# Optimization experiments

Hardware: AMD Instinct MI355X
Metric: run time of the kernel (lower is better)

## Reference

```python
import jax, jax.numpy as jnp
import numpy as np

H = 50      # hidden_size (fixed in source)
IN = 7      # input_size = len(features)
B = 1024    # batch
T = 512     # seq_len
FC1 = 25
OUT = 1


def setup_inputs() -> dict:
    key = jax.random.key(0)
    ks = jax.random.split(key, 24)
    s = 1.0 / np.sqrt(H)  # PyTorch LSTM/Linear default uniform init scale

    def u(k, shape):
        return jax.random.uniform(k, shape, jnp.float32, -s, s)

    d = {"x": jax.random.normal(ks[0], (B, T, IN), jnp.float32)}
    # 4 stacked LSTM layers total: lstm1 has 2 layers (in=7 then 50), lstm2 has 2 layers (in=50)
    in_sizes = [IN, H, H, H]
    for l, isz in enumerate(in_sizes):
        d[f"Wih{l}"] = u(ks[1 + 4 * l], (4 * H, isz))
        d[f"Whh{l}"] = u(ks[2 + 4 * l], (4 * H, H))
        d[f"bih{l}"] = u(ks[3 + 4 * l], (4 * H,))
        d[f"bhh{l}"] = u(ks[4 + 4 * l], (4 * H,))
    d["W1"] = u(ks[17], (FC1, H))
    d["b1"] = u(ks[18], (FC1,))
    d["W2"] = u(ks[19], (OUT, FC1))
    d["b2"] = u(ks[20], (OUT,))
    return d


def _lstm_layer(x, Wih, Whh, bih, bhh):
    # x: [B, T, in] -> hidden sequence [B, T, H]. PyTorch gate order: i, f, g, o.
    b, t, _ = x.shape
    h = Whh.shape[1]
    # Precompute input projection for all timesteps in one big GEMM: [T, B, 4H]
    xp = jnp.einsum('bti,gi->tbg', x, Wih) + (bih + bhh)

    def step(carry, xt):
        hs, cs = carry
        gates = xt + hs @ Whh.T                      # [B, 4H]
        i, f, g, o = jnp.split(gates, 4, axis=-1)
        i = jax.nn.sigmoid(i)
        f = jax.nn.sigmoid(f)
        g = jnp.tanh(g)
        o = jax.nn.sigmoid(o)
        cs = f * cs + i * g
        hs = o * jnp.tanh(cs)
        return (hs, cs), hs

    h0 = jnp.zeros((b, h), x.dtype)
    _, hseq = jax.lax.scan(step, (h0, h0), xp)       # hseq: [T, B, H]
    return hseq.transpose(1, 0, 2)


def reference(x, Wih0, Whh0, bih0, bhh0, Wih1, Whh1, bih1, bhh1,
              Wih2, Whh2, bih2, bhh2, Wih3, Whh3, bih3, bhh3,
              W1, b1, W2, b2):
    out = x
    layers = [(Wih0, Whh0, bih0, bhh0), (Wih1, Whh1, bih1, bhh1),
              (Wih2, Whh2, bih2, bhh2), (Wih3, Whh3, bih3, bhh3)]
    for Wih, Whh, bih, bhh in layers:
        out = _lstm_layer(out, Wih, Whh, bih, bhh)
    h = out[:, -1, :]                                # last timestep [B, H]
    # dropout is identity in eval mode
    h = jax.nn.relu(h @ W1.T + b1)
    return h @ W2.T + b2                             # [B, 1]
```

## Files before the change

### kernel.cpp

```cpp
#include <hip/hip_runtime.h>


#define H 50
#define INSZ 7
#define TT 512
#define NL 4
#define FC1N 25
#define BPG 4
#define NBLK 256
#define NTHREADS 1024
#define HS 80
#define BIASL 56

typedef _Float16 half_t;
typedef __attribute__((ext_vector_type(8))) _Float16 half8_t;
typedef __attribute__((ext_vector_type(4))) float float4_t;

struct Params {
  const float* x;
  const float* Wih[NL];
  const float* Whh[NL];
  const float* bih[NL];
  const float* bhh[NL];
  const float* W1;
  const float* b1;
  const float* W2;
  const float* b2;
  float* out;
};

#define MFMA16(A, B, C) __builtin_amdgcn_mfma_f32_16x16x32_f16((A), (B), (C), 0, 0, 0)
#define EXP2F(x) __builtin_amdgcn_exp2f(x)
#define RCPF(x) __builtin_amdgcn_rcpf(x)

__global__ __launch_bounds__(NTHREADS, 4) void lstm_r13(Params p) {
  __shared__ __align__(16) half_t XP[3][BPG][HS];
  __shared__ __align__(16) half_t Hb[3][3][BPG][HS];
  __shared__ __align__(16) half_t Xstage[32][BPG][8];
  __shared__ int prodc[16];
  __shared__ float fc1_buf[BPG][FC1N];

  const int tid = threadIdx.x;
  const int b0 = blockIdx.x * BPG;
  const int lane = tid & 63;
  const int quad = lane >> 4;
  const int col = lane & 15;
  const int glay = tid >> 8;
  const int wl = (((tid >> 6) & 3) + glay) & 3;

  half8_t afrag[4][4];
#pragma unroll
  for (int t4 = 0; t4 < 4; ++t4) {
#pragma unroll
    for (int g = 0; g < 4; ++g) {
      half8_t v;
#pragma unroll
      for (int j = 0; j < 8; ++j) {
        const int r = wl * 64 + t4 * 16 + col;
        const int u = r >> 2, q = r & 3;
        const int k = g * 32 + quad * 8 + j;
        float wv = 0.0f;
        if (u < H) {
          const int row = q * H + u;
          if (glay == 0) {
            if (k < INSZ) wv = p.Wih[0][row * INSZ + k];
            else if (k == 7) wv = p.bih[0][row] + p.bhh[0][row];
            else if (k >= 8 && k < 8 + H) wv = p.Whh[0][row * H + (k - 8)];
          } else if (glay == 1) {
            if (k == 7) wv = p.bih[1][row] + p.bhh[1][row];
            else if (k >= 8 && k < 8 + H) wv = p.Wih[1][row * H + (k - 8)];
            else if (k >= 64 && k < 64 + H) wv = p.Whh[1][row * H + (k - 64)];
          } else {
            if (k < H) wv = p.Wih[glay][row * H + k];
            else if (k == BIASL) wv = p.bih[glay][row] + p.bhh[glay][row];
            else if (k >= 64 && k < 64 + H) wv = p.Whh[glay][row * H + (k - 64)];
          }
          wv *= (q == 2) ? -2.885390082f : -1.442695041f;
        }
        v[j] = (half_t)wv;
      }
      afrag[t4][g] = v;
    }
  }

  {
    unsigned* xz = (unsigned*)XP;
    for (int i = tid; i < 3 * BPG * HS / 2; i += NTHREADS) xz[i] = 0u;
    unsigned* hz = (unsigned*)Hb;
    for (int i = tid; i < 3 * 3 * BPG * HS / 2; i += NTHREADS) hz[i] = 0u;
    if (tid < 16) prodc[tid] = 0;
  }
  __syncthreads();
  if (tid < 12) {
    XP[tid >> 2][tid & 3][7] = (half_t)1.0f;
  } else if (tid < 12 + 36) {
    const int i = tid - 12, l = i / 12, pr = (i >> 2) % 3, b = i & 3;
    Hb[l][pr][b][BIASL] = (half_t)1.0f;
  }
  for (int i = tid; i < 32 * BPG * INSZ; i += NTHREADS) {
    const int t = i / (BPG * INSZ), rem = i % (BPG * INSZ);
    const int b = rem / INSZ, k = rem % INSZ;
    const half_t xh = (half_t)p.x[((size_t)(b0 + b) * TT + t) * INSZ + k];
    Xstage[t][b][k] = xh;
    if (t == 0) XP[2][b][k] = xh;
  }
  __syncthreads();

  const int bb = col & 3;
  const int tsel = col >> 2;
  const int uu = 16 * wl + 4 * tsel + quad;
  const bool updact = (uu < H);

  const half_t* pin3[3];
  const half_t* pown3[3];
  half_t* pst3[3];
#pragma unroll
  for (int pp = 0; pp < 3; ++pp) {
    if (glay == 0) {
      pin3[pp] = &XP[pp][bb][quad * 8];
      pown3[pp] = pin3[pp];
      pst3[pp] = &XP[pp][bb][8 + uu];
    } else if (glay == 1) {
      pin3[pp] = &XP[pp][bb][quad * 8];
      pown3[pp] = &Hb[0][pp][bb][quad * 8];
      pst3[pp] = &Hb[0][pp][bb][uu];
    } else {
      pin3[pp] = &Hb[glay - 2][pp][bb][quad * 8];
      pown3[pp] = &Hb[glay - 1][pp][bb][quad * 8];
      pst3[pp] = &Hb[glay - 1][pp][bb][uu];
    }
  }
  const half_t* pinT[3] = {glay ? pin3[0] : pin3[2],
                           glay ? pin3[1] : pin3[0],
                           glay ? pin3[2] : pin3[1]};
  const half_t* pownT[3] = {pown3[2], pown3[0], pown3[1]};

  const bool xwave = (glay == 0) && (wl == 3);
  const bool xcopy = xwave && (lane < BPG * INSZ);
  const int cb = lane / INSZ, ck = lane % INSZ;

  float cst = 0.0f;
  const float4_t fzc = {0.0f, 0.0f, 0.0f, 0.0f};
  volatile int* pv = (volatile int*)prodc;

#define WAITT(T_)                                                               \
  {                                                                             \
    const int bS = 4 * (T_);                                                    \
    if (glay == 0) {                                                            \
      while (pv[0] < bS || pv[1] < bS - 4) {}                                   \
    } else if (glay == 1) {                                                     \
      while (pv[1] < bS || pv[0] < bS + 4 || pv[2] < bS - 4) {}                 \
    } else if (glay == 2) {                                                     \
      while (pv[2] < bS || pv[1] < bS + 4 || pv[3] < bS - 4) {}                 \
    } else {                                                                    \
      while (pv[3] < bS || pv[2] < bS + 4) {}                                   \
    }                                                                           \
    __builtin_amdgcn_sched_barrier(0);                                          \
    asm volatile("" ::: "memory");                                              \
  }

#define DONE()                                                                  \
  {                                                                             \
    asm volatile("s_waitcnt lgkmcnt(0)" ::: "memory");                          \
    if (lane == 0) atomicAdd(&prodc[glay], 1);                                  \
  }

#define REFILL(T_)                                                              \
  if (xwave && ((T_)&15) == 0 && (T_) > 0 && (T_) + 16 < TT) {                  \
    const int t0 = (T_) + 16 + (lane >> 2);                                     \
    const int rb = lane & 3;                                                    \
    const float* src = &p.x[((size_t)(b0 + rb) * TT + t0) * INSZ];              \
    half_t* dst = &Xstage[t0 & 31][rb][0];                                      \
    _Pragma("unroll") for (int k = 0; k < INSZ; ++k) dst[k] = (half_t)src[k];   \
  }

#define TICK3(PIN, POWN, PST)                                                   \
  {                                                                             \
    float4_t a0, a1, a2, a3;                                                    \
    if (glay == 0) {                                                            \
      const half8_t v0 = *(const half8_t*)(PIN);                                \
      const half8_t v1 = *(const half8_t*)((PIN) + 32);                         \
      __builtin_amdgcn_s_setprio(1);                                            \
      if (wl != 3) {                                                            \
        a0 = MFMA16(afrag[0][0], v0, fzc); a1 = MFMA16(afrag[1][0], v0, fzc);   \
        a2 = MFMA16(afrag[2][0], v0, fzc); a3 = MFMA16(afrag[3][0], v0, fzc);   \
        a0 = MFMA16(afrag[0][1], v1, a0); a1 = MFMA16(afrag[1][1], v1, a1);     \
        a2 = MFMA16(afrag[2][1], v1, a2); a3 = MFMA16(afrag[3][1], v1, a3);     \
      } else {                                                                  \
        a0 = MFMA16(afrag[0][0], v0, fzc);                                      \
        a0 = MFMA16(afrag[0][1], v1, a0);                                       \
        a1 = a0; a2 = a0; a3 = a0;                                              \
      }                                                                         \
      __builtin_amdgcn_s_setprio(0);                                            \
    } else {                                                                    \
      const half8_t v0 = *(const half8_t*)(PIN);                                \
      const half8_t v1 = *(const half8_t*)((PIN) + 32);                         \
      const half8_t v2 = *(const half8_t*)(POWN);                               \
      const half8_t v3 = *(const half8_t*)((POWN) + 32);                        \
      __builtin_amdgcn_s_setprio(1);                                            \
      if (wl != 3) {                                                            \
        a0 = MFMA16(afrag[0][0], v0, fzc); a1 = MFMA16(afrag[1][0], v0, fzc);   \
        a2 = MFMA16(afrag[2][0], v0, fzc); a3 = MFMA16(afrag[3][0], v0, fzc);   \
        a0 = MFMA16(afrag[0][1], v1, a0); a1 = MFMA16(afrag[1][1], v1, a1);     \
        a2 = MFMA16(afrag[2][1], v1, a2); a3 = MFMA16(afrag[3][1], v1, a3);     \
        a0 = MFMA16(afrag[0][2], v2, a0); a1 = MFMA16(afrag[1][2], v2, a1);     \
        a2 = MFMA16(afrag[2][2], v2, a2); a3 = MFMA16(afrag[3][2], v2, a3);     \
        a0 = MFMA16(afrag[0][3], v3, a0); a1 = MFMA16(afrag[1][3], v3, a1);     \
        a2 = MFMA16(afrag[2][3], v3, a2); a3 = MFMA16(afrag[3][3], v3, a3);     \
      } else {                                                                  \
        a0 = MFMA16(afrag[0][0], v0, fzc);                                      \
        a0 = MFMA16(afrag[0][1], v1, a0);                                       \
        a0 = MFMA16(afrag[0][2], v2, a0);                                       \
        a0 = MFMA16(afrag[0][3], v3, a0);                                       \
        a1 = a0; a2 = a0; a3 = a0;                                              \
      }                                                                         \
      __builtin_amdgcn_s_setprio(0);                                            \
    }                                                                           \
    if (updact) {                                                               \
      const float4_t g01 = (col & 4) ? a1 : a0;                                 \
      const float4_t g23 = (col & 4) ? a3 : a2;                                 \
      const float4_t ga = (col & 8) ? g23 : g01;                                \
      const float di = 1.0f + EXP2F(ga[0]);                                     \
      const float df = 1.0f + EXP2F(ga[1]);                                     \
      const float dg = 1.0f + EXP2F(ga[2]);                                     \
      const float dq = 1.0f + EXP2F(ga[3]);                                     \
      const float r1 = RCPF(di * df);                                           \
      const float r2 = RCPF(dg * dq);                                           \
      const float gi = r1 * df;                                                 \
      const float gf = r1 * di;                                                 \
      const float gg = 2.0f * (r2 * dq) - 1.0f;                                 \
      const float go = r2 * dg;                                                 \
      cst = gf * cst + gi * gg;                                                 \
      const float dc = 1.0f + EXP2F(-2.885390082f * cst);                       \
      const float h = go * (2.0f * RCPF(dc) - 1.0f);                            \
      *(PST) = (half_t)h;                                                       \
    }                                                                           \
  }

#define STEP(T_, P_)                                                            \
  {                                                                             \
    WAITT(T_)                                                                   \
    TICK3(pinT[P_], pownT[P_], pst3[P_])                                        \
    if (xcopy && (T_) + 1 < TT)                                                 \
      XP[P_][cb][ck] = Xstage[((T_) + 1) & 31][cb][ck];                         \
    DONE()                                                                      \
    REFILL(T_)                                                                  \
  }

  for (int T = 0; T < 510; T += 3) {
    STEP(T, 0)
    STEP(T + 1, 1)
    STEP(T + 2, 2)
  }
  STEP(510, 0)
  STEP(511, 1)
  __syncthreads();

  if (tid < BPG * FC1N) {
    const int b = tid / FC1N, j = tid % FC1N;
    const float* w = p.W1 + j * H;
    float a = p.b1[j];
#pragma unroll
    for (int k = 0; k < H; ++k) a += (float)Hb[2][1][b][k] * w[k];
    fc1_buf[b][j] = fmaxf(a, 0.0f);
  }
  __syncthreads();
  if (tid < BPG) {
    float a = p.b2[0];
#pragma unroll
    for (int j = 0; j < FC1N; ++j) a += fc1_buf[tid][j] * p.W2[j];
    p.out[b0 + tid] = a;
  }
}

extern "C" void kernel_launch(void* const* d_in, const int* in_sizes, int n_in,
                              void* d_out, int out_size, void* d_ws, size_t ws_size,
                              hipStream_t stream) {
  Params p;
  p.x = (const float*)d_in[0];
  for (int l = 0; l < NL; ++l) {
    p.Wih[l] = (const float*)d_in[1 + 4 * l];
    p.Whh[l] = (const float*)d_in[2 + 4 * l];
    p.bih[l] = (const float*)d_in[3 + 4 * l];
    p.bhh[l] = (const float*)d_in[4 + 4 * l];
  }
  p.W1 = (const float*)d_in[17];
  p.b1 = (const float*)d_in[18];
  p.W2 = (const float*)d_in[19];
  p.b2 = (const float*)d_in[20];
  p.out = (float*)d_out;

  hipLaunchKernelGGL(lstm_r13, dim3(NBLK), dim3(NTHREADS), 0, stream, p);
}
```

Baseline: 559.9 us.

## Replace atomic-counter spin waits with barrier-phased even/odd layer wavefront schedule

Removes the per-layer shared-memory atomic counters and spin-wait loops. Each timestep slot is now split into two __syncthreads-separated phases, with even and odd layers alternating between MFMA gate computation and the activation/state update, so the layers proceed as a skewed wavefront. The x staging ring grows to 64 steps and is refilled in larger batches. This gets rid of the polling overhead and the atomics, but costs two block-wide barriers per slot and a few extra skew slots.

```diff
diff --git a/kernel.cpp b/kernel.cpp
--- a/kernel.cpp
+++ b/kernel.cpp
@@ -33,11 +33,10 @@
 #define EXP2F(x) __builtin_amdgcn_exp2f(x)
 #define RCPF(x) __builtin_amdgcn_rcpf(x)
 
-__global__ __launch_bounds__(NTHREADS, 4) void lstm_r13(Params p) {
+__global__ __launch_bounds__(NTHREADS, 4) void lstm_r17(Params p) {
   __shared__ __align__(16) half_t XP[3][BPG][HS];
-  __shared__ __align__(16) half_t Hb[3][3][BPG][HS];
-  __shared__ __align__(16) half_t Xstage[32][BPG][8];
-  __shared__ int prodc[16];
+  __shared__ __align__(16) half_t Hbuf[3][3][BPG][HS];
+  __shared__ __align__(16) half_t Xstage[64][BPG][8];
   __shared__ float fc1_buf[BPG][FC1N];
 
   const int tid = threadIdx.x;
@@ -47,6 +46,8 @@
   const int col = lane & 15;
   const int glay = tid >> 8;
   const int wl = (((tid >> 6) & 3) + glay) & 3;
+  const bool isE = ((glay & 1) == 0);
+  const int dl = glay + (glay >> 1);
 
   half8_t afrag[4][4];
 #pragma unroll
@@ -86,18 +87,17 @@
   {
     unsigned* xz = (unsigned*)XP;
     for (int i = tid; i < 3 * BPG * HS / 2; i += NTHREADS) xz[i] = 0u;
-    unsigned* hz = (unsigned*)Hb;
+    unsigned* hz = (unsigned*)Hbuf;
     for (int i = tid; i < 3 * 3 * BPG * HS / 2; i += NTHREADS) hz[i] = 0u;
-    if (tid < 16) prodc[tid] = 0;
   }
   __syncthreads();
   if (tid < 12) {
     XP[tid >> 2][tid & 3][7] = (half_t)1.0f;
   } else if (tid < 12 + 36) {
     const int i = tid - 12, l = i / 12, pr = (i >> 2) % 3, b = i & 3;
-    Hb[l][pr][b][BIASL] = (half_t)1.0f;
-  }
-  for (int i = tid; i < 32 * BPG * INSZ; i += NTHREADS) {
+    Hbuf[l][pr][b][BIASL] = (half_t)1.0f;
+  }
+  for (int i = tid; i < 64 * BPG * INSZ; i += NTHREADS) {
     const int t = i / (BPG * INSZ), rem = i % (BPG * INSZ);
     const int b = rem / INSZ, k = rem % INSZ;
     const half_t xh = (half_t)p.x[((size_t)(b0 + b) * TT + t) * INSZ + k];
@@ -111,75 +111,47 @@
   const int uu = 16 * wl + 4 * tsel + quad;
   const bool updact = (uu < H);
 
-  const half_t* pin3[3];
-  const half_t* pown3[3];
-  half_t* pst3[3];
-#pragma unroll
-  for (int pp = 0; pp < 3; ++pp) {
+  const half_t* inP[3];
+  const half_t* ownP[3];
+  half_t* stP[3];
+#pragma unroll
+  for (int ph = 0; ph < 3; ++ph) {
     if (glay == 0) {
-      pin3[pp] = &XP[pp][bb][quad * 8];
-      pown3[pp] = pin3[pp];
-      pst3[pp] = &XP[pp][bb][8 + uu];
+      inP[ph] = &XP[(ph + 2) % 3][bb][quad * 8];
+      ownP[ph] = inP[ph];
+      stP[ph] = &XP[ph][bb][8 + uu];
     } else if (glay == 1) {
-      pin3[pp] = &XP[pp][bb][quad * 8];
-      pown3[pp] = &Hb[0][pp][bb][quad * 8];
-      pst3[pp] = &Hb[0][pp][bb][uu];
+      inP[ph] = &XP[(ph + 2) % 3][bb][quad * 8];
+      ownP[ph] = &Hbuf[0][(ph + 2) % 3][bb][quad * 8];
+      stP[ph] = &Hbuf[0][ph][bb][uu];
+    } else if (glay == 2) {
+      inP[ph] = &Hbuf[0][(ph + 1) % 3][bb][quad * 8];
+      ownP[ph] = &Hbuf[1][(ph + 2) % 3][bb][quad * 8];
+      stP[ph] = &Hbuf[1][ph][bb][uu];
     } else {
-      pin3[pp] = &Hb[glay - 2][pp][bb][quad * 8];
-      pown3[pp] = &Hb[glay - 1][pp][bb][quad * 8];
-      pst3[pp] = &Hb[glay - 1][pp][bb][uu];
+      inP[ph] = &Hbuf[1][(ph + 2) % 3][bb][quad * 8];
+      ownP[ph] = &Hbuf[2][(ph + 2) % 3][bb][quad * 8];
+      stP[ph] = &Hbuf[2][ph][bb][uu];
     }
   }
-  const half_t* pinT[3] = {glay ? pin3[0] : pin3[2],
-                           glay ? pin3[1] : pin3[0],
-                           glay ? pin3[2] : pin3[1]};
-  const half_t* pownT[3] = {pown3[2], pown3[0], pown3[1]};
 
   const bool xwave = (glay == 0) && (wl == 3);
   const bool xcopy = xwave && (lane < BPG * INSZ);
   const int cb = lane / INSZ, ck = lane % INSZ;
+  const int rb = lane >> 5;
+  const int rt = lane & 31;
 
   float cst = 0.0f;
   const float4_t fzc = {0.0f, 0.0f, 0.0f, 0.0f};
-  volatile int* pv = (volatile int*)prodc;
-
-#define WAITT(T_)                                                               \
+  float4_t a0 = fzc, a1 = fzc, a2 = fzc, a3 = fzc;
+
+#define GUARD(KK) ((unsigned)((KK) - dl) < (unsigned)TT)
+
+#define P1BODY(PIN, POWN)                                                       \
   {                                                                             \
-    const int bS = 4 * (T_);                                                    \
+    const half8_t v0 = *(const half8_t*)(PIN);                                  \
+    const half8_t v1 = *(const half8_t*)((PIN) + 32);                           \
     if (glay == 0) {                                                            \
-      while (pv[0] < bS || pv[1] < bS - 4) {}                                   \
-    } else if (glay == 1) {                                                     \
-      while (pv[1] < bS || pv[0] < bS + 4 || pv[2] < bS - 4) {}                 \
-    } else if (glay == 2) {                                                     \
-      while (pv[2] < bS || pv[1] < bS + 4 || pv[3] < bS - 4) {}                 \
-    } else {                                                                    \
-      while (pv[3] < bS || pv[2] < bS + 4) {}                                   \
-    }                                                                           \
-    __builtin_amdgcn_sched_barrier(0);                                          \
-    asm volatile("" ::: "memory");                                              \
-  }
-
-#define DONE()                                                                  \
-  {                                                                             \
-    asm volatile("s_waitcnt lgkmcnt(0)" ::: "memory");                          \
-    if (lane == 0) atomicAdd(&prodc[glay], 1);                                  \
-  }
-
-#define REFILL(T_)                                                              \
-  if (xwave && ((T_)&15) == 0 && (T_) > 0 && (T_) + 16 < TT) {                  \
-    const int t0 = (T_) + 16 + (lane >> 2);                                     \
-    const int rb = lane & 3;                                                    \
-    const float* src = &p.x[((size_t)(b0 + rb) * TT + t0) * INSZ];              \
-    half_t* dst = &Xstage[t0 & 31][rb][0];                                      \
-    _Pragma("unroll") for (int k = 0; k < INSZ; ++k) dst[k] = (half_t)src[k];   \
-  }
-
-#define TICK3(PIN, POWN, PST)                                                   \
-  {                                                                             \
-    float4_t a0, a1, a2, a3;                                                    \
-    if (glay == 0) {                                                            \
-      const half8_t v0 = *(const half8_t*)(PIN);                                \
-      const half8_t v1 = *(const half8_t*)((PIN) + 32);                         \
       __builtin_amdgcn_s_setprio(1);                                            \
       if (wl != 3) {                                                            \
         a0 = MFMA16(afrag[0][0], v0, fzc); a1 = MFMA16(afrag[1][0], v0, fzc);   \
@@ -193,8 +165,6 @@
       }                                                                         \
       __builtin_amdgcn_s_setprio(0);                                            \
     } else {                                                                    \
-      const half8_t v0 = *(const half8_t*)(PIN);                                \
-      const half8_t v1 = *(const half8_t*)((PIN) + 32);                         \
       const half8_t v2 = *(const half8_t*)(POWN);                               \
       const half8_t v3 = *(const half8_t*)((POWN) + 32);                        \
       __builtin_amdgcn_s_setprio(1);                                            \
@@ -216,44 +186,71 @@
       }                                                                         \
       __builtin_amdgcn_s_setprio(0);                                            \
     }                                                                           \
-    if (updact) {                                                               \
-      const float4_t g01 = (col & 4) ? a1 : a0;                                 \
-      const float4_t g23 = (col & 4) ? a3 : a2;                                 \
-      const float4_t ga = (col & 8) ? g23 : g01;                                \
-      const float di = 1.0f + EXP2F(ga[0]);                                     \
-      const float df = 1.0f + EXP2F(ga[1]);                                     \
-      const float dg = 1.0f + EXP2F(ga[2]);                                     \
-      const float dq = 1.0f + EXP2F(ga[3]);                                     \
-      const float r1 = RCPF(di * df);                                           \
-      const float r2 = RCPF(dg * dq);                                           \
-      const float gi = r1 * df;                                                 \
-      const float gf = r1 * di;                                                 \
-      const float gg = 2.0f * (r2 * dq) - 1.0f;                                 \
-      const float go = r2 * dg;                                                 \
-      cst = gf * cst + gi * gg;                                                 \
-      const float dc = 1.0f + EXP2F(-2.885390082f * cst);                       \
-      const float h = go * (2.0f * RCPF(dc) - 1.0f);                            \
-      *(PST) = (half_t)h;                                                       \
-    }                                                                           \
-  }
-
-#define STEP(T_, P_)                                                            \
+  }
+
+#define P2BODY(PST)                                                             \
+  if (updact) {                                                                 \
+    const float4_t g01 = (col & 4) ? a1 : a0;                                   \
+    const float4_t g23 = (col & 4) ? a3 : a2;                                   \
+    const float4_t ga = (col & 8) ? g23 : g01;                                  \
+    const float di = 1.0f + EXP2F(ga[0]);                                       \
+    const float df = 1.0f + EXP2F(ga[1]);                                       \
+    const float dg = 1.0f + EXP2F(ga[2]);                                       \
+    const float dq = 1.0f + EXP2F(ga[3]);                                       \
+    const float r1 = RCPF(di * df);                                             \
+    const float r2 = RCPF(dg * dq);                                             \
+    const float gi = r1 * df;                                                   \
+    const float gf = r1 * di;                                                   \
+    const float gg = 2.0f * (r2 * dq) - 1.0f;                                   \
+    const float go = r2 * dg;                                                   \
+    cst = gf * cst + gi * gg;                                                   \
+    const float dc = 1.0f + EXP2F(-2.885390082f * cst);                         \
+    const float h = go * (2.0f * RCPF(dc) - 1.0f);                              \
+    *(PST) = (half_t)h;                                                         \
+  }
+
+#define REFILL(K_)                                                              \
+  if (xwave && ((K_)&31) == 8 && (K_) < 480) {                                  \
+    const int tb = ((K_) & ~31) + 32;                                           \
+    _Pragma("unroll") for (int pp = 0; pp < 2; ++pp) {                          \
+      const int b = rb + 2 * pp;                                                \
+      const int t = tb + rt;                                                    \
+      const float* src = &p.x[((size_t)(b0 + b) * TT + t) * INSZ];              \
+      half_t* dst = &Xstage[t & 63][b][0];                                      \
+      _Pragma("unroll") for (int kk = 0; kk < INSZ; ++kk)                       \
+          dst[kk] = (half_t)src[kk];                                            \
+    }                                                                           \
+  }
+
+#define SLOT(K_, PH)                                                            \
   {                                                                             \
-    WAITT(T_)                                                                   \
-    TICK3(pinT[P_], pownT[P_], pst3[P_])                                        \
-    if (xcopy && (T_) + 1 < TT)                                                 \
-      XP[P_][cb][ck] = Xstage[((T_) + 1) & 31][cb][ck];                         \
-    DONE()                                                                      \
-    REFILL(T_)                                                                  \
-  }
-
-  for (int T = 0; T < 510; T += 3) {
-    STEP(T, 0)
-    STEP(T + 1, 1)
-    STEP(T + 2, 2)
-  }
-  STEP(510, 0)
-  STEP(511, 1)
+    if (isE) {                                                                  \
+      if (GUARD(K_)) P1BODY(inP[PH], ownP[PH])                                  \
+    } else {                                                                    \
+      if (GUARD((K_)-1)) P2BODY(stP[((PH) + 2) % 3])                            \
+    }                                                                           \
+    __syncthreads();                                                            \
+    if (isE) {                                                                  \
+      if (GUARD(K_)) {                                                          \
+        REFILL(K_)                                                              \
+        P2BODY(stP[PH])                                                         \
+        if (xcopy && (K_) + 1 < TT)                                             \
+          XP[PH][cb][ck] = Xstage[((K_) + 1) & 63][cb][ck];                     \
+      }                                                                         \
+    } else {                                                                    \
+      if (GUARD(K_)) P1BODY(inP[PH], ownP[PH])                                  \
+    }                                                                           \
+    __syncthreads();                                                            \
+  }
+
+  for (int k = 0; k < 516; k += 3) {
+    SLOT(k, 0)
+    SLOT(k + 1, 1)
+    SLOT(k + 2, 2)
+  }
+  if (!isE && GUARD(515)) {
+    P2BODY(stP[2])
+  }
   __syncthreads();
 
   if (tid < BPG * FC1N) {
@@ -261,7 +258,7 @@
     const float* w = p.W1 + j * H;
     float a = p.b1[j];
 #pragma unroll
-    for (int k = 0; k < H; ++k) a += (float)Hb[2][1][b][k] * w[k];
+    for (int k = 0; k < H; ++k) a += (float)Hbuf[2][2][b][k] * w[k];
     fc1_buf[b][j] = fmaxf(a, 0.0f);
   }
   __syncthreads();
@@ -290,5 +287,5 @@
   p.b2 = (const float*)d_in[20];
   p.out = (float*)d_out;
 
-  hipLaunchKernelGGL(lstm_r13, dim3(NBLK), dim3(NTHREADS), 0, stream, p);
+  hipLaunchKernelGGL(lstm_r17, dim3(NBLK), dim3(NTHREADS), 0, stream, p);
 }
```

After: 570.6 us. Within noise of the previous version (+1.9%).
